# Optimization experiments

Hardware: AMD Instinct MI355X
Metric: run time of the kernel (lower is better)

## Reference

```python
import jax, jax.numpy as jnp
import numpy as np


def _parallel_scan_affine(log_a, b):
    """Hillis-Steele doubling scan for h_t = a_t*h_{t-1} + b_t (h_0 = 0).

    log_a, b: (B, T, d). Operator: (la2,b2) o (la1,b1) = (la1+la2, exp(la2)*b1 + b2).
    """
    T = log_a.shape[1]
    la, bv = log_a, b
    stride = 1
    while stride < T:  # static Python loop, log2(T) rounds
        la_prev = jnp.roll(la, stride, axis=1).at[:, :stride, :].set(0.0)
        bv_prev = jnp.roll(bv, stride, axis=1).at[:, :stride, :].set(0.0)
        bv = jnp.exp(la) * bv_prev + bv
        la = la + la_prev
        stride *= 2
    return bv


def setup_inputs() -> dict:
    key = jax.random.key(0)
    kx, kwz, kwh = jax.random.split(key, 3)
    B, T, D = 4, 4096, 1024
    x = jax.random.normal(kx, (B, T, D), dtype=jnp.float32)
    # nn.Linear(D, D) weights, stored as (out, in) like torch
    Wz = jax.random.normal(kwz, (D, D), dtype=jnp.float32) * 0.02
    bz = jnp.zeros((D,), dtype=jnp.float32)
    Wh = jax.random.normal(kwh, (D, D), dtype=jnp.float32) * 0.02
    bh = jnp.zeros((D,), dtype=jnp.float32)
    return {"x": x, "Wz": Wz, "bz": bz, "Wh": Wh, "bh": bh}


def reference(x, Wz, bz, Wh, bh):
    # forward_parallel: z = sigmoid(linear_z(x)); h_tilde = linear_h(x)
    z = jax.nn.sigmoid(jnp.einsum("btd,ed->bte", x, Wz) + bz)
    h_tilde = jnp.einsum("btd,ed->bte", x, Wh) + bh
    log_a = jnp.log(1.0 - z + 1e-08)
    b = z * h_tilde
    h_out = _parallel_scan_affine(log_a, b)
    return h_out  # out_proj is Identity since d_inner == d_model
```

## Files before the change

kernel.cpp:

```cpp
#include <hip/hip_runtime.h>
#include <hip/hip_bf16.h>


typedef __bf16 bf16x8 __attribute__((ext_vector_type(8)));
typedef __bf16 bf16x4 __attribute__((ext_vector_type(4)));
typedef float  f32x4  __attribute__((ext_vector_type(4)));

#define BSZ 4
#define TSZ 4096
#define DSZ 1024
#define MSZ (BSZ*TSZ)
#define CH  16
#define NC  (TSZ/CH)

__device__ __forceinline__ void gload_lds16(const __bf16* g, __bf16* l) {
  __builtin_amdgcn_global_load_lds(
      (const __attribute__((address_space(1))) void*)g,
      (__attribute__((address_space(3))) void*)l, 16, 0, 0);
}

__global__ void convert_tile_kernel(const float* __restrict__ X,
                                    const float* __restrict__ Wz,
                                    const float* __restrict__ Wh,
                                    __bf16* __restrict__ Xc,
                                    __bf16* __restrict__ Wzc,
                                    __bf16* __restrict__ Whc)
{
  const int bx = blockIdx.x;
  const float* src; __bf16* dst; int gid;
  if (bx < 8192)      { src = X;  dst = Xc;  gid =  bx        *256 + threadIdx.x; }
  else if (bx < 8704) { src = Wz; dst = Wzc; gid = (bx - 8192)*256 + threadIdx.x; }
  else                { src = Wh; dst = Whc; gid = (bx - 8704)*256 + threadIdx.x; }
  const int l    = gid & 63;
  const int i    = (gid >> 6) & 7;
  const int kblk = (gid >> 9) & 31;
  const int rblk = gid >> 14;
  const int row  = rblk*128 + i*16 + (l & 15);
  const int col  = kblk*32 + (l >> 4)*8;
  const float* g = src + (size_t)row*DSZ + col;
  float4 v0 = *(const float4*)g;
  float4 v1 = *(const float4*)(g + 4);
  bf16x8 p;
  p[0]=(__bf16)v0.x; p[1]=(__bf16)v0.y; p[2]=(__bf16)v0.z; p[3]=(__bf16)v0.w;
  p[4]=(__bf16)v1.x; p[5]=(__bf16)v1.y; p[6]=(__bf16)v1.z; p[7]=(__bf16)v1.w;
  *(bf16x8*)(dst + (size_t)gid*8) = p;
}

__global__ __launch_bounds__(256, 2) void gemm_gate_kernel(
    const __bf16* __restrict__ Xc,  const __bf16* __restrict__ Wzc,
    const __bf16* __restrict__ Whc,
    const float* __restrict__ bz, const float* __restrict__ bh,
    __bf16* __restrict__ a_ws, float* __restrict__ b_out,
    float* __restrict__ Aprod, float* __restrict__ Bcomp)
{
  __shared__ __align__(16) __bf16 As [8192];
  __shared__ __align__(16) __bf16 Bzs[8192];
  __shared__ __align__(16) __bf16 Bhs[8192];

  const int tid  = threadIdx.x;
  const int lane = tid & 63;
  const int wv   = tid >> 6;
  const int wM   = (wv >> 1) * 64;
  const int wN   = (wv & 1) * 64;
  const int wMg  = wM >> 4;
  const int wNg  = wN >> 4;
  const int lr   = lane & 15;
  const int q    = lane >> 4;
  const int wbase = wv * 64;

  const __bf16* Xb = Xc  + (size_t)blockIdx.x * 32 * 4096;
  const __bf16* Zb = Wzc + (size_t)blockIdx.y * 32 * 4096;
  const __bf16* Hb = Whc + (size_t)blockIdx.y * 32 * 4096;

  f32x4 accz[4][4] = {};
  f32x4 acch[4][4] = {};

  for (int kblk = 0; kblk < 16; ++kblk) {
    __syncthreads();
    const size_t tb = (size_t)kblk * 8192;
    #pragma unroll
    for (int c = 0; c < 4; ++c) {
      const int eo = (c*256 + wbase + lane) * 8;
      const int lo = (c*256 + wbase) * 8;
      gload_lds16(Xb + tb + eo, As  + lo);
      gload_lds16(Zb + tb + eo, Bzs + lo);
      gload_lds16(Hb + tb + eo, Bhs + lo);
    }
    __syncthreads();

    #pragma unroll
    for (int h = 0; h < 2; ++h) {
      const int ho = h * 4096;
      bf16x8 af[4];
      #pragma unroll
      for (int i = 0; i < 4; ++i)
        af[i] = *(const bf16x8*)(As + ho + (wMg + i)*512 + lane*8);
      #pragma unroll
      for (int j = 0; j < 4; ++j) {
        bf16x8 bz8 = *(const bf16x8*)(Bzs + ho + (wNg + j)*512 + lane*8);
        bf16x8 bh8 = *(const bf16x8*)(Bhs + ho + (wNg + j)*512 + lane*8);
        #pragma unroll
        for (int i = 0; i < 4; ++i) {
          accz[j][i] = __builtin_amdgcn_mfma_f32_16x16x32_bf16(af[i], bz8, accz[j][i], 0, 0, 0);
          acch[j][i] = __builtin_amdgcn_mfma_f32_16x16x32_bf16(af[i], bh8, acch[j][i], 0, 0, 0);
        }
      }
    }
  }

  const int M0 = blockIdx.x * 128;
  const int N0 = blockIdx.y * 128;
  #pragma unroll
  for (int j = 0; j < 4; ++j) {
    const int e = N0 + wN + j*16 + lr;
    const float bzv = bz[e];
    const float bhv = bh[e];
    float Aseg[4], Bseg[4];
    #pragma unroll
    for (int i = 0; i < 4; ++i) {
      const int mbase = M0 + wM + i*16 + q*4;
      float A = 1.0f, Bv = 0.0f;
      #pragma unroll
      for (int r = 0; r < 4; ++r) {
        const size_t idx = (size_t)(mbase + r)*DSZ + e;
        const float pz = accz[j][i][r] + bzv;
        const float ph = acch[j][i][r] + bhv;
        const float ex = __expf(-pz);
        const float z  = 1.0f / (1.0f + ex);
        const __bf16 abf = (__bf16)fmaf(ex, z, 1e-8f);
        const float  af  = (float)abf;
        const float  bf  = z * ph;
        a_ws[idx]  = abf;
        b_out[idx] = bf;
        Bv = fmaf(af, Bv, bf);
        A *= af;
      }
      Aseg[i] = A; Bseg[i] = Bv;
    }
    #pragma unroll
    for (int i = 0; i < 4; ++i) {
      #pragma unroll
      for (int s = 16; s < 64; s <<= 1) {
        const float Ap = __shfl_up(Aseg[i], s, 64);
        const float Bp = __shfl_up(Bseg[i], s, 64);
        if (lane >= s) { Bseg[i] = fmaf(Aseg[i], Bp, Bseg[i]); Aseg[i] *= Ap; }
      }
    }
    if (q == 3) {
      #pragma unroll
      for (int i = 0; i < 4; ++i) {
        const int bc = (M0 + wM + i*16) >> 4;
        Aprod[(size_t)bc*DSZ + e] = Aseg[i];
        Bcomp[(size_t)bc*DSZ + e] = Bseg[i];
      }
    }
  }
}

__global__ void scan_pass2_kernel(const float* Aprod,
                                  const float* __restrict__ Bcomp,
                                  float* Hstart)
{
  const int lane = threadIdx.x & 63;
  const int wave = (blockIdx.x * 256 + threadIdx.x) >> 6;
  const int b = wave >> 10;
  const int d = wave & 1023;
  const size_t i0 = (size_t)(b*NC + 4*lane)*DSZ + d;
  float Ac[4], Bc[4];
  #pragma unroll
  for (int c = 0; c < 4; ++c) {
    Ac[c] = Aprod[i0 + (size_t)c*DSZ];
    Bc[c] = Bcomp[i0 + (size_t)c*DSZ];
  }
  float A = Ac[0], Bv = Bc[0];
  #pragma unroll
  for (int c = 1; c < 4; ++c) { Bv = fmaf(Ac[c], Bv, Bc[c]); A *= Ac[c]; }
  #pragma unroll
  for (int s = 1; s < 64; s <<= 1) {
    const float Ap = __shfl_up(A,  s, 64);
    const float Bp = __shfl_up(Bv, s, 64);
    if (lane >= s) { Bv = fmaf(A, Bp, Bv); A *= Ap; }
  }
  float h = __shfl_up(Bv, 1, 64);
  if (lane == 0) h = 0.0f;
  #pragma unroll
  for (int c = 0; c < 4; ++c) {
    Hstart[i0 + (size_t)c*DSZ] = h;
    h = fmaf(Ac[c], h, Bc[c]);
  }
}

__global__ void scan_pass3_kernel(const __bf16* __restrict__ a_ws,
                                  const float* __restrict__ Hstart,
                                  float* __restrict__ out)
{
  const int bc   = blockIdx.x;
  const int d0   = threadIdx.x * 4;
  const size_t base = (size_t)bc * CH * DSZ + d0;
  float4 hv = *(const float4*)(Hstart + (size_t)bc*DSZ + d0);
  float h[4] = {hv.x, hv.y, hv.z, hv.w};
  #pragma unroll
  for (int t = 0; t < CH; ++t) {
    bf16x4 a4 = *(const bf16x4*)(a_ws + base + (size_t)t*DSZ);
    float4 b4 = *(const float4*)(out + base + (size_t)t*DSZ);
    const float bb[4] = {b4.x, b4.y, b4.z, b4.w};
    #pragma unroll
    for (int c = 0; c < 4; ++c)
      h[c] = fmaf((float)a4[c], h[c], bb[c]);
    *(float4*)(out + base + (size_t)t*DSZ) = make_float4(h[0], h[1], h[2], h[3]);
  }
}

extern "C" void kernel_launch(void* const* d_in, const int* in_sizes, int n_in,
                              void* d_out, int out_size, void* d_ws, size_t ws_size,
                              hipStream_t stream)
{
  const float* x  = (const float*)d_in[0];
  const float* Wz = (const float*)d_in[1];
  const float* bz = (const float*)d_in[2];
  const float* Wh = (const float*)d_in[3];
  const float* bh = (const float*)d_in[4];
  float* out = (float*)d_out;

  __bf16* Xc   = (__bf16*)d_ws;
  __bf16* Wzc  = Xc  + (size_t)MSZ * DSZ;
  __bf16* Whc  = Wzc + (size_t)DSZ * DSZ;
  __bf16* a_ws = Whc + (size_t)DSZ * DSZ;
  float* Aprod  = (float*)(a_ws + (size_t)MSZ * DSZ);
  float* Bcomp  = Aprod + (size_t)BSZ*NC*DSZ;
  float* Hstart = Aprod;

  convert_tile_kernel<<<9216, 256, 0, stream>>>(x, Wz, Wh, Xc, Wzc, Whc);
  gemm_gate_kernel<<<dim3(MSZ/128, DSZ/128), 256, 0, stream>>>(
      Xc, Wzc, Whc, bz, bh, a_ws, out, Aprod, Bcomp);
  scan_pass2_kernel<<<(BSZ*DSZ)/4, 256, 0, stream>>>(Aprod, Bcomp, Hstart);
  scan_pass3_kernel<<<BSZ*NC, 256, 0, stream>>>(a_ws, Hstart, out);
}
```

Before: 256.3 us.

## Replace wave-parallel chunk-prefix scan with sequential per-channel scan in pass2

The second scan pass no longer runs a shuffle-based parallel prefix over chunk summaries. Each thread now owns one (batch, channel) pair and walks all 256 chunk summaries serially, loading them in batches of 16 with coalesced access across channels. This removes the strided, uncoalesced loads and the shuffle work of the old version. In exchange the launch shrinks to 64 blocks of 64 threads, which leaves most compute units idle and puts 16 dependent load rounds on the critical path.

```diff
diff --git a/kernel.cpp b/kernel.cpp
--- a/kernel.cpp
+++ b/kernel.cpp
@@ -157,36 +157,28 @@
   }
 }
 
+#define P2B 16
 __global__ void scan_pass2_kernel(const float* Aprod,
                                   const float* __restrict__ Bcomp,
                                   float* Hstart)
 {
   const int lane = threadIdx.x & 63;
-  const int wave = (blockIdx.x * 256 + threadIdx.x) >> 6;
-  const int b = wave >> 10;
-  const int d = wave & 1023;
-  const size_t i0 = (size_t)(b*NC + 4*lane)*DSZ + d;
-  float Ac[4], Bc[4];
-  #pragma unroll
-  for (int c = 0; c < 4; ++c) {
-    Ac[c] = Aprod[i0 + (size_t)c*DSZ];
-    Bc[c] = Bcomp[i0 + (size_t)c*DSZ];
-  }
-  float A = Ac[0], Bv = Bc[0];
-  #pragma unroll
-  for (int c = 1; c < 4; ++c) { Bv = fmaf(Ac[c], Bv, Bc[c]); A *= Ac[c]; }
-  #pragma unroll
-  for (int s = 1; s < 64; s <<= 1) {
-    const float Ap = __shfl_up(A,  s, 64);
-    const float Bp = __shfl_up(Bv, s, 64);
-    if (lane >= s) { Bv = fmaf(A, Bp, Bv); A *= Ap; }
-  }
-  float h = __shfl_up(Bv, 1, 64);
-  if (lane == 0) h = 0.0f;
-  #pragma unroll
-  for (int c = 0; c < 4; ++c) {
-    Hstart[i0 + (size_t)c*DSZ] = h;
-    h = fmaf(Ac[c], h, Bc[c]);
+  const int b    = blockIdx.x >> 4;
+  const int d    = (blockIdx.x & 15) * 64 + lane;
+  const size_t base = (size_t)b * NC * DSZ + d;
+  float h = 0.0f;
+  for (int c0 = 0; c0 < NC; c0 += P2B) {
+    float Ar[P2B], Br[P2B];
+    #pragma unroll
+    for (int c = 0; c < P2B; ++c) {
+      Ar[c] = Aprod[base + (size_t)(c0 + c)*DSZ];
+      Br[c] = Bcomp[base + (size_t)(c0 + c)*DSZ];
+    }
+    #pragma unroll
+    for (int c = 0; c < P2B; ++c) {
+      Hstart[base + (size_t)(c0 + c)*DSZ] = h;
+      h = fmaf(Ar[c], h, Br[c]);
+    }
   }
 }
 
@@ -233,6 +225,6 @@
   convert_tile_kernel<<<9216, 256, 0, stream>>>(x, Wz, Wh, Xc, Wzc, Whc);
   gemm_gate_kernel<<<dim3(MSZ/128, DSZ/128), 256, 0, stream>>>(
       Xc, Wzc, Whc, bz, bh, a_ws, out, Aprod, Bcomp);
-  scan_pass2_kernel<<<(BSZ*DSZ)/4, 256, 0, stream>>>(Aprod, Bcomp, Hstart);
+  scan_pass2_kernel<<<64, 64, 0, stream>>>(Aprod, Bcomp, Hstart);
   scan_pass3_kernel<<<BSZ*NC, 256, 0, stream>>>(a_ws, Hstart, out);
 }
```

Measured after the change: 241.3 us. 1.06x faster.
